# Kernel optimization log

Hardware: AMD Instinct MI355X
Metric: run time of the kernel (lower is better)

The kernel has to match this reference:

```python
import jax, jax.numpy as jnp
import numpy as np

B, S, D = 16, 2048, 64
SCALE = 1.0 / np.sqrt(np.float32(D))  # forward divides by sqrt(embedding_dim=64)


def setup_inputs() -> dict:
    key = jax.random.key(0)
    ks = jax.random.split(key, 7)
    return {
        "x": jax.random.normal(ks[0], (B, S, D), dtype=jnp.float32),
        "Wq": jax.random.normal(ks[1], (D, D), dtype=jnp.float32) * 0.02,
        "bq": jax.random.normal(ks[2], (D,), dtype=jnp.float32) * 0.02,
        "Wk": jax.random.normal(ks[3], (D, D), dtype=jnp.float32) * 0.02,
        "bk": jax.random.normal(ks[4], (D,), dtype=jnp.float32) * 0.02,
        "Wv": jax.random.normal(ks[5], (D, D), dtype=jnp.float32) * 0.02,
        "bv": jax.random.normal(ks[6], (D,), dtype=jnp.float32) * 0.02,
    }


def reference(x, Wq, bq, Wk, bk, Wv, bv):
    # Linear projections (weights stored [in, out], math-equivalent to nn.Linear)
    q = jnp.einsum("bsd,de->bse", x, Wq) + bq
    k = jnp.einsum("bsd,de->bse", x, Wk) + bk
    v = jnp.einsum("bsd,de->bse", x, Wv) + bv
    # Unfused scores: [B, S, S]
    scores = jnp.einsum("bqd,bkd->bqk", q, k) * jnp.float32(SCALE)
    causal = jnp.tril(jnp.ones((S, S), dtype=bool))  # mask[:S,:S]
    scores = jnp.where(causal, scores, jnp.float32(-jnp.inf))
    attn = jax.nn.softmax(scores, axis=-1)
    # dropout is identity in eval mode (reference baseline)
    out = jnp.einsum("bqk,bkd->bqd", attn, v)
    return out
```

## Files before the change

kernel.cpp:

```cpp
#include <hip/hip_runtime.h>

#define NB 16
#define SS 2048
#define DD 64

typedef __attribute__((ext_vector_type(8))) short short8;
typedef __attribute__((ext_vector_type(4))) float f32x4;

#define SCL2E 0.18033688011112042f

__device__ __forceinline__ short f2bf(float f) {
  union { float f; unsigned u; } v; v.f = f;
  unsigned r = (v.u + 0x7fffu + ((v.u >> 16) & 1u)) >> 16;
  return (short)r;
}

__device__ __forceinline__ unsigned cvtpk_bf16(float lo, float hi) {
  unsigned r;
  asm("v_cvt_pk_bf16_f32 %0, %1, %2" : "=v"(r) : "v"(lo), "v"(hi));
  return r;
}

__device__ __forceinline__ short8 load_a_frag_f32(const float* p) {
  float4 u = *(const float4*)p;
  float4 w = *(const float4*)(p + 4);
  short8 r;
  r[0] = f2bf(u.x); r[1] = f2bf(u.y); r[2] = f2bf(u.z); r[3] = f2bf(u.w);
  r[4] = f2bf(w.x); r[5] = f2bf(w.y); r[6] = f2bf(w.z); r[7] = f2bf(w.w);
  return r;
}

__global__ __launch_bounds__(768) void proj_kernel(
    const float* __restrict__ x,
    const float* __restrict__ Wq, const float* __restrict__ bq,
    const float* __restrict__ Wk, const float* __restrict__ bk,
    const float* __restrict__ Wv, const float* __restrict__ bv,
    ushort* __restrict__ qo, ushort* __restrict__ ko, ushort* __restrict__ vT)
{
  __shared__ __align__(16) ushort Wt[3][64][72];
  __shared__ __align__(16) ushort Vs[64][68];
  const int t = threadIdx.x;
#pragma unroll
  for (int i = 0; i < 4; ++i) {
    int idx = i * 3072 + t * 4;
    int m = idx >> 12, rem = idx & 4095;
    int kk = rem >> 6, n0 = rem & 63;
    const float* src = (m == 0 ? Wq : (m == 1 ? Wk : Wv));
    float4 w4 = *(const float4*)(src + rem);
    Wt[m][n0 + 0][kk] = (ushort)f2bf(w4.x);
    Wt[m][n0 + 1][kk] = (ushort)f2bf(w4.y);
    Wt[m][n0 + 2][kk] = (ushort)f2bf(w4.z);
    Wt[m][n0 + 3][kk] = (ushort)f2bf(w4.w);
  }
  __syncthreads();

  const int lane = t & 63, w = t >> 6;
  const int l15 = lane & 15, quad = lane >> 4;
  const int mm = w >> 2, rr = w & 3;
  const int g = blockIdx.x * 64 + rr * 16 + l15;

  short8 b0 = load_a_frag_f32(x + (size_t)g * 64 + quad * 8);
  short8 b1 = load_a_frag_f32(x + (size_t)g * 64 + 32 + quad * 8);

  const float* bp = (mm == 0 ? bq : (mm == 1 ? bk : bv));
  ushort* outp = (mm == 0 ? qo : ko);

#pragma unroll
  for (int nt = 0; nt < 4; ++nt) {
    short8 a0 = *(const short8*)&Wt[mm][nt * 16 + l15][quad * 8];
    short8 a1 = *(const short8*)&Wt[mm][nt * 16 + l15][32 + quad * 8];
    f32x4 acc = {0.f, 0.f, 0.f, 0.f};
    acc = __builtin_amdgcn_mfma_f32_16x16x32_bf16(a0, b0, acc, 0, 0, 0);
    acc = __builtin_amdgcn_mfma_f32_16x16x32_bf16(a1, b1, acc, 0, 0, 0);
    float4 bb = *(const float4*)(bp + nt * 16 + quad * 4);
    uint2 pk;
    pk.x = cvtpk_bf16(acc[0] + bb.x, acc[1] + bb.y);
    pk.y = cvtpk_bf16(acc[2] + bb.z, acc[3] + bb.w);
    if (mm == 2) {
      *(uint2*)&Vs[rr * 16 + l15][nt * 16 + quad * 4] = pk;
    } else {
      *(uint2*)(outp + (size_t)g * 64 + nt * 16 + quad * 4) = pk;
    }
  }
  __syncthreads();
  if (t < 256) {
    const int batch = blockIdx.x >> 5;
    const int s0 = (blockIdx.x & 31) * 64;
    const int d = t >> 2, j0 = (t & 3) * 16;
    ushort tmp[16];
#pragma unroll
    for (int j = 0; j < 16; ++j) tmp[j] = Vs[j0 + j][d];
    ushort* dst = vT + (size_t)batch * DD * SS + (size_t)d * SS + s0 + j0;
    ((int4*)dst)[0] = ((int4*)tmp)[0];
    ((int4*)dst)[1] = ((int4*)tmp)[1];
  }
}

__device__ __forceinline__ short8 build_pa(unsigned A0, unsigned A1,
                                           unsigned B0, unsigned B1, int quad) {
  int xA0 = __shfl_xor((int)A0, 32);
  int xA1 = __shfl_xor((int)A1, 32);
  int xB0 = __shfl_xor((int)B0, 32);
  int xB1 = __shfl_xor((int)B1, 32);
  const bool hi = quad >= 2;
  const bool odd = quad & 1;
  int Lo0 = hi ? xB0 : (int)A0;
  int Lo1 = hi ? xB1 : (int)A1;
  int Hi0 = hi ? (int)B0 : xA0;
  int Hi1 = hi ? (int)B1 : xA1;
  int xLo0 = __shfl_xor(Lo0, 16);
  int xLo1 = __shfl_xor(Lo1, 16);
  int xHi0 = __shfl_xor(Hi0, 16);
  int xHi1 = __shfl_xor(Hi1, 16);
  int4 wv;
  wv.x = odd ? xHi0 : Lo0;
  wv.y = odd ? xHi1 : Lo1;
  wv.z = odd ? Hi0 : xLo0;
  wv.w = odd ? Hi1 : xLo1;
  return *(short8*)&wv;
}

template<bool MASKED>
__device__ __forceinline__ void attn_half(
    const f32x4 (&c)[4], float& l_acc, f32x4 (&acc)[4],
    const short8 (&vf0)[4], const short8 (&vf1)[4],
    int keybase, int qabs, int quad)
{
  unsigned pk[4][2];
#pragma unroll
  for (int ct = 0; ct < 4; ++ct) {
    float pe[4];
#pragma unroll
    for (int r = 0; r < 4; ++r) {
      float p = __builtin_amdgcn_exp2f(c[ct][r] * SCL2E);
      if (MASKED && (keybase + ct * 16 + quad * 4 + r > qabs)) p = 0.f;
      pe[r] = p;
      l_acc += p;
    }
    pk[ct][0] = cvtpk_bf16(pe[0], pe[1]);
    pk[ct][1] = cvtpk_bf16(pe[2], pe[3]);
  }
  short8 pa0 = build_pa(pk[0][0], pk[0][1], pk[1][0], pk[1][1], quad);
  short8 pa1 = build_pa(pk[2][0], pk[2][1], pk[3][0], pk[3][1], quad);
  __builtin_amdgcn_s_setprio(1);
#pragma unroll
  for (int nt = 0; nt < 4; ++nt) {
    acc[nt] = __builtin_amdgcn_mfma_f32_16x16x32_bf16(pa0, vf0[nt], acc[nt], 0, 0, 0);
    acc[nt] = __builtin_amdgcn_mfma_f32_16x16x32_bf16(pa1, vf1[nt], acc[nt], 0, 0, 0);
  }
  __builtin_amdgcn_s_setprio(0);
}

struct KFrag { short8 f0[4]; short8 f1[4]; };

__device__ __forceinline__ void load_k(KFrag& K, const ushort* kp0,
                                       const ushort* kp1) {
  K.f0[0] = *(const short8*)(kp0);
  K.f1[0] = *(const short8*)(kp0 + 32);
  K.f0[1] = *(const short8*)(kp0 + 1024);
  K.f1[1] = *(const short8*)(kp0 + 1056);
  K.f0[2] = *(const short8*)(kp1);
  K.f1[2] = *(const short8*)(kp1 + 32);
  K.f0[3] = *(const short8*)(kp1 + 1024);
  K.f1[3] = *(const short8*)(kp1 + 1056);
}

template<bool MASKED>
__device__ __forceinline__ void tile_compute(
    const KFrag& K,
    const ushort* vp0, const ushort* vp1, const ushort* vp2, const ushort* vp3,
    const short8& a0, const short8& a1, const short8& a2, const short8& a3,
    f32x4 (&acc0)[4], f32x4 (&acc1)[4], float& l0, float& l1,
    int kb, int qabs0, int qabs1, int quad)
{
  short8 vf0[4], vf1[4];
  vf0[0] = *(const short8*)(vp0); vf1[0] = *(const short8*)(vp0 + 32);
  vf0[1] = *(const short8*)(vp1); vf1[1] = *(const short8*)(vp1 + 32);
  vf0[2] = *(const short8*)(vp2); vf1[2] = *(const short8*)(vp2 + 32);
  vf0[3] = *(const short8*)(vp3); vf1[3] = *(const short8*)(vp3 + 32);

  f32x4 c0[4], c1[4];
  __builtin_amdgcn_s_setprio(1);
#pragma unroll
  for (int ct = 0; ct < 4; ++ct) {
    f32x4 z = {0.f, 0.f, 0.f, 0.f};
    c0[ct] = __builtin_amdgcn_mfma_f32_16x16x32_bf16(K.f0[ct], a0, z, 0, 0, 0);
    c0[ct] = __builtin_amdgcn_mfma_f32_16x16x32_bf16(K.f1[ct], a1, c0[ct], 0, 0, 0);
    c1[ct] = __builtin_amdgcn_mfma_f32_16x16x32_bf16(K.f0[ct], a2, z, 0, 0, 0);
    c1[ct] = __builtin_amdgcn_mfma_f32_16x16x32_bf16(K.f1[ct], a3, c1[ct], 0, 0, 0);
  }
  __builtin_amdgcn_s_setprio(0);

  attn_half<MASKED>(c0, l0, acc0, vf0, vf1, kb, qabs0, quad);
  attn_half<MASKED>(c1, l1, acc1, vf0, vf1, kb, qabs1, quad);
}

__global__ __launch_bounds__(256, 2) void attn_kernel(
    const ushort* __restrict__ qg, const ushort* __restrict__ kg,
    const ushort* __restrict__ vT, float* __restrict__ out)
{
  __shared__ __align__(16) float accW[2][32][68];
  __shared__ float lW[4][32];

  const int t = threadIdx.x, bid = blockIdx.x;
  const int batch = (bid & 7) * 2 + ((bid >> 3) & 1);
  const int qt = 63 - (bid >> 4);
  const int q0 = qt * 32;
  const int lane = t & 63, w = t >> 6;
  const int l15 = lane & 15, quad = lane >> 4;
  const size_t bbase = (size_t)batch * SS * DD;

  const ushort* qp = qg + bbase + (size_t)(q0 + l15) * 64 + quad * 8;
  short8 a0 = *(const short8*)qp;
  short8 a1 = *(const short8*)(qp + 32);
  short8 a2 = *(const short8*)(qp + 16 * 64);
  short8 a3 = *(const short8*)(qp + 16 * 64 + 32);

  f32x4 acc0[4], acc1[4];
  float l0 = 0.f, l1 = 0.f;
#pragma unroll
  for (int nt = 0; nt < 4; ++nt) {
    acc0[nt] = (f32x4){0.f, 0.f, 0.f, 0.f};
    acc1[nt] = (f32x4){0.f, 0.f, 0.f, 0.f};
  }

  const int ktotal = ((q0 + 31) >> 6) + 1;
  const ushort* kp0 = kg + bbase + (size_t)(w * 64 + l15) * 64 + quad * 8;
  const ushort* kp1 = kp0 + 2048;
  const ushort* vp0 = vT + bbase + (size_t)(l15) * SS + w * 64 + quad * 8;
  const ushort* vp1 = vp0 + 16 * SS;
  const ushort* vp2 = vp0 + 32 * SS;
  const ushort* vp3 = vp0 + 48 * SS;

  const int qabs0 = q0 + l15, qabs1 = q0 + 16 + l15;

  int kt = w;
  if (kt < ktotal) {
    KFrag KA, KB;
    load_k(KA, kp0, kp1);
    kp0 += 16384; kp1 += 16384;
    while (true) {
      int ktn = kt + 4;
      if (ktn < ktotal) { load_k(KB, kp0, kp1); kp0 += 16384; kp1 += 16384; }
      if (kt == ktotal - 1)
        tile_compute<true >(KA, vp0, vp1, vp2, vp3, a0, a1, a2, a3,
                            acc0, acc1, l0, l1, kt * 64, qabs0, qabs1, quad);
      else
        tile_compute<false>(KA, vp0, vp1, vp2, vp3, a0, a1, a2, a3,
                            acc0, acc1, l0, l1, kt * 64, qabs0, qabs1, quad);
      vp0 += 256; vp1 += 256; vp2 += 256; vp3 += 256;
      if (ktn >= ktotal) break;
      kt = ktn;
      ktn = kt + 4;
      if (ktn < ktotal) { load_k(KA, kp0, kp1); kp0 += 16384; kp1 += 16384; }
      if (kt == ktotal - 1)
        tile_compute<true >(KB, vp0, vp1, vp2, vp3, a0, a1, a2, a3,
                            acc0, acc1, l0, l1, kt * 64, qabs0, qabs1, quad);
      else
        tile_compute<false>(KB, vp0, vp1, vp2, vp3, a0, a1, a2, a3,
                            acc0, acc1, l0, l1, kt * 64, qabs0, qabs1, quad);
      vp0 += 256; vp1 += 256; vp2 += 256; vp3 += 256;
      if (ktn >= ktotal) break;
      kt = ktn;
    }
  }

  l0 += __shfl_xor(l0, 16); l0 += __shfl_xor(l0, 32);
  l1 += __shfl_xor(l1, 16); l1 += __shfl_xor(l1, 32);

  if (lane < 16) {
    lW[w][lane] = l0;
    lW[w][16 + lane] = l1;
  }
  if (w < 2) {
#pragma unroll
    for (int r = 0; r < 4; ++r)
#pragma unroll
      for (int nt = 0; nt < 4; ++nt) {
        accW[w][quad * 4 + r][nt * 16 + l15] = acc0[nt][r];
        accW[w][16 + quad * 4 + r][nt * 16 + l15] = acc1[nt][r];
      }
  }
  __syncthreads();
  if (w >= 2) {
#pragma unroll
    for (int r = 0; r < 4; ++r)
#pragma unroll
      for (int nt = 0; nt < 4; ++nt) {
        accW[w - 2][quad * 4 + r][nt * 16 + l15] += acc0[nt][r];
        accW[w - 2][16 + quad * 4 + r][nt * 16 + l15] += acc1[nt][r];
      }
  }
  __syncthreads();

  {
    const int row = t >> 3, col0 = (t & 7) * 8;
    float den = lW[0][row] + lW[1][row] + lW[2][row] + lW[3][row];
    float iv = 1.0f / den;
    float4 oa, ob;
    {
      float4 x0 = *(const float4*)&accW[0][row][col0];
      float4 x1 = *(const float4*)&accW[0][row][col0 + 4];
      float4 y0 = *(const float4*)&accW[1][row][col0];
      float4 y1 = *(const float4*)&accW[1][row][col0 + 4];
      oa.x = x0.x + y0.x; oa.y = x0.y + y0.y; oa.z = x0.z + y0.z; oa.w = x0.w + y0.w;
      ob.x = x1.x + y1.x; ob.y = x1.y + y1.y; ob.z = x1.z + y1.z; ob.w = x1.w + y1.w;
    }
    oa.x *= iv; oa.y *= iv; oa.z *= iv; oa.w *= iv;
    ob.x *= iv; ob.y *= iv; ob.z *= iv; ob.w *= iv;
    float* op = out + bbase + (size_t)(q0 + row) * 64 + col0;
    *(float4*)op = oa;
    *(float4*)(op + 4) = ob;
  }
}

extern "C" void kernel_launch(void* const* d_in, const int* in_sizes, int n_in,
                              void* d_out, int out_size, void* d_ws, size_t ws_size,
                              hipStream_t stream) {
  (void)in_sizes; (void)n_in; (void)out_size; (void)ws_size;
  const float* x  = (const float*)d_in[0];
  const float* Wq = (const float*)d_in[1];
  const float* bq = (const float*)d_in[2];
  const float* Wk = (const float*)d_in[3];
  const float* bk = (const float*)d_in[4];
  const float* Wv = (const float*)d_in[5];
  const float* bv = (const float*)d_in[6];
  float* out = (float*)d_out;

  ushort* qws = (ushort*)d_ws;
  ushort* kws = qws + (size_t)NB * SS * DD;
  ushort* vws = kws + (size_t)NB * SS * DD;

  proj_kernel<<<dim3(NB * SS / 64), dim3(768), 0, stream>>>(
      x, Wq, bq, Wk, bk, Wv, bv, qws, kws, vws);
  attn_kernel<<<dim3(NB * (SS / 32)), dim3(256), 0, stream>>>(
      qws, kws, vws, out);
}
```

Baseline: 118.9 us.

## Split attention by query rows per wave instead of key tiles, tile V layout

The attention kernel now gives each wave its own 16 query rows of a 64-row block and loops over all key tiles itself. This removes the cross-wave LDS reduction and the two block barriers, and each wave writes its output directly. V is stored in per-64-key tiles of 64x64 so V fragments load contiguously. The trade-offs are that waves in a block now have unequal causal work, the software double-buffering of K is dropped, the grid is halved, and the output stores become scalar and strided.

```diff
diff --git a/kernel.cpp b/kernel.cpp
--- a/kernel.cpp
+++ b/kernel.cpp
@@ -35,7 +35,7 @@
     const float* __restrict__ Wq, const float* __restrict__ bq,
     const float* __restrict__ Wk, const float* __restrict__ bk,
     const float* __restrict__ Wv, const float* __restrict__ bv,
-    ushort* __restrict__ qo, ushort* __restrict__ ko, ushort* __restrict__ vT)
+    ushort* __restrict__ qo, ushort* __restrict__ ko, ushort* __restrict__ vt)
 {
   __shared__ __align__(16) ushort Wt[3][64][72];
   __shared__ __align__(16) ushort Vs[64][68];
@@ -85,12 +85,12 @@
   __syncthreads();
   if (t < 256) {
     const int batch = blockIdx.x >> 5;
-    const int s0 = (blockIdx.x & 31) * 64;
+    const int ktile = blockIdx.x & 31;
     const int d = t >> 2, j0 = (t & 3) * 16;
     ushort tmp[16];
 #pragma unroll
     for (int j = 0; j < 16; ++j) tmp[j] = Vs[j0 + j][d];
-    ushort* dst = vT + (size_t)batch * DD * SS + (size_t)d * SS + s0 + j0;
+    ushort* dst = vt + (size_t)batch * SS * DD + ktile * 4096 + d * 64 + j0;
     ((int4*)dst)[0] = ((int4*)tmp)[0];
     ((int4*)dst)[1] = ((int4*)tmp)[1];
   }
@@ -151,166 +151,75 @@
   __builtin_amdgcn_s_setprio(0);
 }
 
-struct KFrag { short8 f0[4]; short8 f1[4]; };
-
-__device__ __forceinline__ void load_k(KFrag& K, const ushort* kp0,
-                                       const ushort* kp1) {
-  K.f0[0] = *(const short8*)(kp0);
-  K.f1[0] = *(const short8*)(kp0 + 32);
-  K.f0[1] = *(const short8*)(kp0 + 1024);
-  K.f1[1] = *(const short8*)(kp0 + 1056);
-  K.f0[2] = *(const short8*)(kp1);
-  K.f1[2] = *(const short8*)(kp1 + 32);
-  K.f0[3] = *(const short8*)(kp1 + 1024);
-  K.f1[3] = *(const short8*)(kp1 + 1056);
-}
-
-template<bool MASKED>
-__device__ __forceinline__ void tile_compute(
-    const KFrag& K,
-    const ushort* vp0, const ushort* vp1, const ushort* vp2, const ushort* vp3,
-    const short8& a0, const short8& a1, const short8& a2, const short8& a3,
-    f32x4 (&acc0)[4], f32x4 (&acc1)[4], float& l0, float& l1,
-    int kb, int qabs0, int qabs1, int quad)
+__global__ __launch_bounds__(256) void attn_kernel(
+    const ushort* __restrict__ qg, const ushort* __restrict__ kg,
+    const ushort* __restrict__ vt, float* __restrict__ out)
 {
-  short8 vf0[4], vf1[4];
-  vf0[0] = *(const short8*)(vp0); vf1[0] = *(const short8*)(vp0 + 32);
-  vf0[1] = *(const short8*)(vp1); vf1[1] = *(const short8*)(vp1 + 32);
-  vf0[2] = *(const short8*)(vp2); vf1[2] = *(const short8*)(vp2 + 32);
-  vf0[3] = *(const short8*)(vp3); vf1[3] = *(const short8*)(vp3 + 32);
-
-  f32x4 c0[4], c1[4];
-  __builtin_amdgcn_s_setprio(1);
-#pragma unroll
-  for (int ct = 0; ct < 4; ++ct) {
-    f32x4 z = {0.f, 0.f, 0.f, 0.f};
-    c0[ct] = __builtin_amdgcn_mfma_f32_16x16x32_bf16(K.f0[ct], a0, z, 0, 0, 0);
-    c0[ct] = __builtin_amdgcn_mfma_f32_16x16x32_bf16(K.f1[ct], a1, c0[ct], 0, 0, 0);
-    c1[ct] = __builtin_amdgcn_mfma_f32_16x16x32_bf16(K.f0[ct], a2, z, 0, 0, 0);
-    c1[ct] = __builtin_amdgcn_mfma_f32_16x16x32_bf16(K.f1[ct], a3, c1[ct], 0, 0, 0);
-  }
-  __builtin_amdgcn_s_setprio(0);
-
-  attn_half<MASKED>(c0, l0, acc0, vf0, vf1, kb, qabs0, quad);
-  attn_half<MASKED>(c1, l1, acc1, vf0, vf1, kb, qabs1, quad);
-}
-
-__global__ __launch_bounds__(256, 2) void attn_kernel(
-    const ushort* __restrict__ qg, const ushort* __restrict__ kg,
-    const ushort* __restrict__ vT, float* __restrict__ out)
-{
-  __shared__ __align__(16) float accW[2][32][68];
-  __shared__ float lW[4][32];
-
   const int t = threadIdx.x, bid = blockIdx.x;
   const int batch = (bid & 7) * 2 + ((bid >> 3) & 1);
-  const int qt = 63 - (bid >> 4);
-  const int q0 = qt * 32;
+  const int qt = 31 - (bid >> 4);
   const int lane = t & 63, w = t >> 6;
   const int l15 = lane & 15, quad = lane >> 4;
+  const int qrow0 = qt * 64 + w * 16;
   const size_t bbase = (size_t)batch * SS * DD;
 
-  const ushort* qp = qg + bbase + (size_t)(q0 + l15) * 64 + quad * 8;
+  const ushort* qp = qg + bbase + (size_t)(qrow0 + l15) * 64 + quad * 8;
   short8 a0 = *(const short8*)qp;
   short8 a1 = *(const short8*)(qp + 32);
-  short8 a2 = *(const short8*)(qp + 16 * 64);
-  short8 a3 = *(const short8*)(qp + 16 * 64 + 32);
-
-  f32x4 acc0[4], acc1[4];
-  float l0 = 0.f, l1 = 0.f;
-#pragma unroll
-  for (int nt = 0; nt < 4; ++nt) {
-    acc0[nt] = (f32x4){0.f, 0.f, 0.f, 0.f};
-    acc1[nt] = (f32x4){0.f, 0.f, 0.f, 0.f};
-  }
-
-  const int ktotal = ((q0 + 31) >> 6) + 1;
-  const ushort* kp0 = kg + bbase + (size_t)(w * 64 + l15) * 64 + quad * 8;
-  const ushort* kp1 = kp0 + 2048;
-  const ushort* vp0 = vT + bbase + (size_t)(l15) * SS + w * 64 + quad * 8;
-  const ushort* vp1 = vp0 + 16 * SS;
-  const ushort* vp2 = vp0 + 32 * SS;
-  const ushort* vp3 = vp0 + 48 * SS;
-
-  const int qabs0 = q0 + l15, qabs1 = q0 + 16 + l15;
-
-  int kt = w;
-  if (kt < ktotal) {
-    KFrag KA, KB;
-    load_k(KA, kp0, kp1);
-    kp0 += 16384; kp1 += 16384;
-    while (true) {
-      int ktn = kt + 4;
-      if (ktn < ktotal) { load_k(KB, kp0, kp1); kp0 += 16384; kp1 += 16384; }
-      if (kt == ktotal - 1)
-        tile_compute<true >(KA, vp0, vp1, vp2, vp3, a0, a1, a2, a3,
-                            acc0, acc1, l0, l1, kt * 64, qabs0, qabs1, quad);
-      else
-        tile_compute<false>(KA, vp0, vp1, vp2, vp3, a0, a1, a2, a3,
-                            acc0, acc1, l0, l1, kt * 64, qabs0, qabs1, quad);
-      vp0 += 256; vp1 += 256; vp2 += 256; vp3 += 256;
-      if (ktn >= ktotal) break;
-      kt = ktn;
-      ktn = kt + 4;
-      if (ktn < ktotal) { load_k(KA, kp0, kp1); kp0 += 16384; kp1 += 16384; }
-      if (kt == ktotal - 1)
-        tile_compute<true >(KB, vp0, vp1, vp2, vp3, a0, a1, a2, a3,
-                            acc0, acc1, l0, l1, kt * 64, qabs0, qabs1, quad);
-      else
-        tile_compute<false>(KB, vp0, vp1, vp2, vp3, a0, a1, a2, a3,
-                            acc0, acc1, l0, l1, kt * 64, qabs0, qabs1, quad);
-      vp0 += 256; vp1 += 256; vp2 += 256; vp3 += 256;
-      if (ktn >= ktotal) break;
-      kt = ktn;
+
+  f32x4 acc[4];
+  float l0 = 0.f;
+#pragma unroll
+  for (int nt = 0; nt < 4; ++nt) acc[nt] = (f32x4){0.f, 0.f, 0.f, 0.f};
+
+  const int ktot = ((qrow0 + 15) >> 6) + 1;
+  const ushort* kpA = kg + bbase + l15 * 64 + quad * 8;
+  const ushort* kpB = kpA + 2048;
+  const ushort* vpA = vt + bbase + l15 * 64 + quad * 8;
+  const ushort* vpB = vpA + 2048;
+  const int qabs = qrow0 + l15;
+
+  for (int kt = 0; kt < ktot; ++kt) {
+    short8 kf0[4], kf1[4], vf0[4], vf1[4];
+    kf0[0] = *(const short8*)(kpA);        kf1[0] = *(const short8*)(kpA + 32);
+    kf0[1] = *(const short8*)(kpA + 1024); kf1[1] = *(const short8*)(kpA + 1056);
+    kf0[2] = *(const short8*)(kpB);        kf1[2] = *(const short8*)(kpB + 32);
+    kf0[3] = *(const short8*)(kpB + 1024); kf1[3] = *(const short8*)(kpB + 1056);
+    vf0[0] = *(const short8*)(vpA);        vf1[0] = *(const short8*)(vpA + 32);
+    vf0[1] = *(const short8*)(vpA + 1024); vf1[1] = *(const short8*)(vpA + 1056);
+    vf0[2] = *(const short8*)(vpB);        vf1[2] = *(const short8*)(vpB + 32);
+    vf0[3] = *(const short8*)(vpB + 1024); vf1[3] = *(const short8*)(vpB + 1056);
+
+    f32x4 c[4];
+    __builtin_amdgcn_s_setprio(1);
+#pragma unroll
+    for (int ct = 0; ct < 4; ++ct) {
+      f32x4 z = {0.f, 0.f, 0.f, 0.f};
+      c[ct] = __builtin_amdgcn_mfma_f32_16x16x32_bf16(kf0[ct], a0, z, 0, 0, 0);
+      c[ct] = __builtin_amdgcn_mfma_f32_16x16x32_bf16(kf1[ct], a1, c[ct], 0, 0, 0);
     }
-  }
-
-  l0 += __shfl_xor(l0, 16); l0 += __shfl_xor(l0, 32);
-  l1 += __shfl_xor(l1, 16); l1 += __shfl_xor(l1, 32);
-
-  if (lane < 16) {
-    lW[w][lane] = l0;
-    lW[w][16 + lane] = l1;
-  }
-  if (w < 2) {
-#pragma unroll
-    for (int r = 0; r < 4; ++r)
-#pragma unroll
-      for (int nt = 0; nt < 4; ++nt) {
-        accW[w][quad * 4 + r][nt * 16 + l15] = acc0[nt][r];
-        accW[w][16 + quad * 4 + r][nt * 16 + l15] = acc1[nt][r];
-      }
-  }
-  __syncthreads();
-  if (w >= 2) {
-#pragma unroll
-    for (int r = 0; r < 4; ++r)
-#pragma unroll
-      for (int nt = 0; nt < 4; ++nt) {
-        accW[w - 2][quad * 4 + r][nt * 16 + l15] += acc0[nt][r];
-        accW[w - 2][16 + quad * 4 + r][nt * 16 + l15] += acc1[nt][r];
-      }
-  }
-  __syncthreads();
-
-  {
-    const int row = t >> 3, col0 = (t & 7) * 8;
-    float den = lW[0][row] + lW[1][row] + lW[2][row] + lW[3][row];
+    __builtin_amdgcn_s_setprio(0);
+
+    if (kt == ktot - 1)
+      attn_half<true >(c, l0, acc, vf0, vf1, kt * 64, qabs, quad);
+    else
+      attn_half<false>(c, l0, acc, vf0, vf1, kt * 64, qabs, quad);
+
+    kpA += 4096; kpB += 4096; vpA += 4096; vpB += 4096;
+  }
+
+  l0 += __shfl_xor(l0, 16);
+  l0 += __shfl_xor(l0, 32);
+
+  float* ob = out + bbase;
+#pragma unroll
+  for (int r = 0; r < 4; ++r) {
+    float den = __shfl(l0, quad * 4 + r);
     float iv = 1.0f / den;
-    float4 oa, ob;
-    {
-      float4 x0 = *(const float4*)&accW[0][row][col0];
-      float4 x1 = *(const float4*)&accW[0][row][col0 + 4];
-      float4 y0 = *(const float4*)&accW[1][row][col0];
-      float4 y1 = *(const float4*)&accW[1][row][col0 + 4];
-      oa.x = x0.x + y0.x; oa.y = x0.y + y0.y; oa.z = x0.z + y0.z; oa.w = x0.w + y0.w;
-      ob.x = x1.x + y1.x; ob.y = x1.y + y1.y; ob.z = x1.z + y1.z; ob.w = x1.w + y1.w;
-    }
-    oa.x *= iv; oa.y *= iv; oa.z *= iv; oa.w *= iv;
-    ob.x *= iv; ob.y *= iv; ob.z *= iv; ob.w *= iv;
-    float* op = out + bbase + (size_t)(q0 + row) * 64 + col0;
-    *(float4*)op = oa;
-    *(float4*)(op + 4) = ob;
+    float* orow = ob + (size_t)(qrow0 + quad * 4 + r) * 64 + l15;
+#pragma unroll
+    for (int nt = 0; nt < 4; ++nt)
+      orow[nt * 16] = acc[nt][r] * iv;
   }
 }
 
@@ -333,6 +242,6 @@
 
   proj_kernel<<<dim3(NB * SS / 64), dim3(768), 0, stream>>>(
       x, Wq, bq, Wk, bk, Wv, bv, qws, kws, vws);
-  attn_kernel<<<dim3(NB * (SS / 32)), dim3(256), 0, stream>>>(
+  attn_kernel<<<dim3(NB * (SS / 64)), dim3(256), 0, stream>>>(
       qws, kws, vws, out);
 }
```

Result: slower. 167.3 us (+40.8%).
